# Performance work log

Measured on AMD Instinct MI355X. Metric: run time of the kernel, lower is better.

## Reference

```python
import jax, jax.numpy as jnp
from jax import lax
import numpy as np

B, F, T, D, H = 16, 20, 128, 300, 256

def _lstm_scan(x, mask, W, U, b):
    # x: [N, T, D], mask: [N, T] bool. Keras gate order: i, f, g(c), o.
    N = x.shape[0]
    xz = jnp.einsum('ntd,dh->nth', x, W) + b  # [N, T, 4H] input projection, hoisted out of scan
    def step(carry, inp):
        h, c = carry
        z_x, m = inp
        z = z_x + h @ U
        i, f, g, o = jnp.split(z, 4, axis=-1)
        c_new = jax.nn.sigmoid(f) * c + jax.nn.sigmoid(i) * jnp.tanh(g)
        h_new = jax.nn.sigmoid(o) * jnp.tanh(c_new)
        m = m[:, None]
        # Keras masking: masked steps copy previous state/output through
        h = jnp.where(m, h_new, h)
        c = jnp.where(m, c_new, c)
        return (h, c), h
    init = (jnp.zeros((N, H), x.dtype), jnp.zeros((N, H), x.dtype))
    _, hs = lax.scan(step, init, (jnp.swapaxes(xz, 0, 1), jnp.swapaxes(mask, 0, 1)))
    return jnp.swapaxes(hs, 0, 1)  # [N, T, H]

def setup_inputs() -> dict:
    key = jax.random.key(0)
    ks = jax.random.split(key, 8)
    facts = jax.random.normal(ks[0], (B, F, T, D), dtype=jnp.float32)
    lengths = jax.random.randint(ks[1], (B, F), T // 2, T + 1)
    mask = jnp.arange(T)[None, None, :] < lengths[..., None]  # valid-prefix padding mask [B,F,T]
    s_in = 1.0 / np.sqrt(D)
    s_h = 1.0 / np.sqrt(H)
    W_fwd = jax.random.normal(ks[2], (D, 4 * H), dtype=jnp.float32) * s_in
    U_fwd = jax.random.normal(ks[3], (H, 4 * H), dtype=jnp.float32) * s_h
    b_fwd = jnp.zeros((4 * H,), dtype=jnp.float32).at[H:2 * H].set(1.0)  # unit forget bias
    W_bwd = jax.random.normal(ks[4], (D, 4 * H), dtype=jnp.float32) * s_in
    U_bwd = jax.random.normal(ks[5], (H, 4 * H), dtype=jnp.float32) * s_h
    b_bwd = jnp.zeros((4 * H,), dtype=jnp.float32).at[H:2 * H].set(1.0)
    return {"facts": facts, "mask": mask, "W_fwd": W_fwd, "U_fwd": U_fwd, "b_fwd": b_fwd,
            "W_bwd": W_bwd, "U_bwd": U_bwd, "b_bwd": b_bwd}

def reference(facts, mask, W_fwd, U_fwd, b_fwd, W_bwd, U_bwd, b_bwd):
    # Flatten (B, F) -> N sequences, as in FactEncoder.call
    x = facts.reshape(B * F, T, D)
    m = mask.reshape(B * F, T)
    h_f = _lstm_scan(x, m, W_fwd, U_fwd, b_fwd)
    # Bidirectional backward branch: reverse time, run, reverse output back
    h_b = _lstm_scan(x[:, ::-1], m[:, ::-1], W_bwd, U_bwd, b_bwd)[:, ::-1]
    out = jnp.concatenate([h_f, h_b], axis=-1)  # merge_mode='concat'
    return out.reshape(B, F, T, 2 * H)
```

## Files before the change

### kernel.cpp

```cpp
#include <hip/hip_runtime.h>
#include <hip/hip_bf16.h>

constexpr int Bc   = 16;
constexpr int Fc   = 20;
constexpr int T    = 128;
constexpr int D    = 300;
constexpr int H    = 256;
constexpr int NSEQ = Bc * Fc;
constexpr int G4   = 4 * H;
constexpr int DP   = 320;

constexpr int WTN = 2 * G4 * DP;
constexpr int UTN = 2 * G4 * H;

typedef __attribute__((ext_vector_type(8))) short  short8_t;
typedef __attribute__((ext_vector_type(4))) float  f32x4;

__device__ __forceinline__ short8_t ld8(const short* p) { return *(const short8_t*)p; }
__device__ __forceinline__ f32x4 mf(short8_t a, short8_t b, f32x4 c) {
    return __builtin_amdgcn_mfma_f32_16x16x32_bf16(a, b, c, 0, 0, 0);
}
__device__ __forceinline__ float b2f(short s) {
    unsigned u = ((unsigned)(unsigned short)s) << 16;
    return __builtin_bit_cast(float, u);
}
__device__ __forceinline__ short f2b(float f) {
    unsigned u = __builtin_bit_cast(unsigned, f);
    u += 0x7fffu + ((u >> 16) & 1u);
    return (short)(u >> 16);
}
__device__ __forceinline__ float blo(unsigned w) { return __builtin_bit_cast(float, w << 16); }
__device__ __forceinline__ float bhi(unsigned w) { return __builtin_bit_cast(float, w & 0xffff0000u); }
__device__ __forceinline__ float sigf(float x) {
    float e = __builtin_amdgcn_exp2f(x * -1.44269504f);
    return __builtin_amdgcn_rcpf(1.0f + e);
}
__device__ __forceinline__ float tanhf_(float x) {
    float e = __builtin_amdgcn_exp2f(x * -2.88539008f);
    return __builtin_amdgcn_rcpf(1.0f + e) * 2.0f - 1.0f;
}
__device__ __forceinline__ bool in_is_fp32(const unsigned* bfw) {
    return bfw[256] == 0x3F800000u;
}
__device__ __forceinline__ float in_val(const void* p, long long i, bool is32) {
    return is32 ? ((const float*)p)[i] : b2f(((const short*)p)[i]);
}

__global__ void prep_wu(const void* __restrict__ Wf, const void* __restrict__ Uf,
                        const void* __restrict__ Wb, const void* __restrict__ Ub,
                        const unsigned* __restrict__ bfw,
                        short* __restrict__ wt, short* __restrict__ ut)
{
    const bool is32 = in_is_fp32(bfw);
    int idx = blockIdx.x * 256 + threadIdx.x;
    if (idx < WTN) {
        int d_ = idx / (G4 * DP), j = idx - d_ * (G4 * DP);
        int n  = j / DP, k = j - n * DP;
        const void* W = d_ ? Wb : Wf;
        wt[idx] = (k < D) ? f2b(in_val(W, (long long)k * G4 + n, is32)) : (short)0;
    } else if (idx < WTN + UTN) {
        int i  = idx - WTN;
        int d_ = i / (G4 * H), j = i - d_ * (G4 * H);
        int n  = j / H, k = j - n * H;
        const void* U = d_ ? Ub : Uf;
        int kp = (k & ~31) | ((k & 15) << 1) | ((k >> 4) & 1);
        ut[i - k + kp] = f2b(in_val(U, (long long)k * G4 + n, is32));
    }
}

__global__ void prep_xp(const void* __restrict__ facts, const unsigned* __restrict__ bfw,
                        short* __restrict__ xpc, int Tc, int t00, int t01, int ndir)
{
    const bool is32 = in_is_fp32(bfw);
    long long total = (long long)ndir * NSEQ * Tc * DP;
    long long idx = (long long)blockIdx.x * 256 + threadIdx.x;
    if (idx >= total) return;
    int perdir = NSEQ * Tc * DP;
    int d_  = (int)(idx / perdir);
    int rem = (int)(idx - (long long)d_ * perdir);
    int seq = rem / (Tc * DP);
    int r2  = rem - seq * (Tc * DP);
    int tl  = r2 / DP;
    int k   = r2 - tl * DP;
    int t0  = d_ ? t01 : t00;
    long long frow = (long long)(seq * T + t0 + tl) * D;
    xpc[idx] = (k < D) ? f2b(in_val(facts, frow + k, is32)) : (short)0;
}

__global__ void gemm_xz(const short* __restrict__ xpc, const short* __restrict__ wt,
                        const void* __restrict__ bfv, const void* __restrict__ bbv,
                        const unsigned* __restrict__ bfw,
                        short* __restrict__ xzc, int Tc, int aDirStride)
{
    const bool is32 = in_is_fp32(bfw);
    const int dir = blockIdx.z;
    const short* wtd  = wt + (size_t)dir * G4 * DP;
    const void*  bias = dir ? bbv : bfv;
    const short* xpA = xpc + (size_t)dir * aDirStride + (size_t)blockIdx.y * 128 * DP;
    short* xzd = xzc + (size_t)dir * NSEQ * Tc * G4;

    const int m0 = blockIdx.y * 128;
    const int n0 = blockIdx.x * 128;
    const int tid = threadIdx.x;
    const int wid = tid >> 6, lane = tid & 63, quad = lane >> 4, l15 = lane & 15;
    const int wm = wid >> 1, wn = wid & 1;

    __shared__ __align__(16) short Al[128 * 40];
    __shared__ __align__(16) short Bl[128 * 40];

    const short* wtB = wtd + (size_t)n0 * DP;

    const int row0 = tid >> 2,          cc0 = tid & 3;
    const int row1 = (tid + 256) >> 2,  cc1 = (tid + 256) & 3;

    f32x4 acc[4][4];
#pragma unroll
    for (int mi = 0; mi < 4; ++mi)
#pragma unroll
        for (int ni = 0; ni < 4; ++ni) acc[mi][ni] = (f32x4){0.f, 0.f, 0.f, 0.f};

    short8_t ra0, ra1, rb0, rb1;
    ra0 = ld8(xpA + (size_t)row0 * DP + cc0 * 8);
    rb0 = ld8(wtB + (size_t)row0 * DP + cc0 * 8);
    ra1 = ld8(xpA + (size_t)row1 * DP + cc1 * 8);
    rb1 = ld8(wtB + (size_t)row1 * DP + cc1 * 8);

    for (int kk = 0; kk < 10; ++kk) {
        __syncthreads();
        *(short8_t*)&Al[row0 * 40 + cc0 * 8] = ra0;
        *(short8_t*)&Bl[row0 * 40 + cc0 * 8] = rb0;
        *(short8_t*)&Al[row1 * 40 + cc1 * 8] = ra1;
        *(short8_t*)&Bl[row1 * 40 + cc1 * 8] = rb1;
        __syncthreads();

        if (kk < 9) {
            int ko = (kk + 1) * 32;
            ra0 = ld8(xpA + (size_t)row0 * DP + ko + cc0 * 8);
            rb0 = ld8(wtB + (size_t)row0 * DP + ko + cc0 * 8);
            ra1 = ld8(xpA + (size_t)row1 * DP + ko + cc1 * 8);
            rb1 = ld8(wtB + (size_t)row1 * DP + ko + cc1 * 8);
        }

        short8_t a[4], b[4];
#pragma unroll
        for (int mi = 0; mi < 4; ++mi)
            a[mi] = ld8(&Al[(wm * 64 + mi * 16 + l15) * 40 + quad * 8]);
#pragma unroll
        for (int ni = 0; ni < 4; ++ni)
            b[ni] = ld8(&Bl[(wn * 64 + ni * 16 + l15) * 40 + quad * 8]);
#pragma unroll
        for (int mi = 0; mi < 4; ++mi)
#pragma unroll
            for (int ni = 0; ni < 4; ++ni)
                acc[mi][ni] = mf(a[mi], b[ni], acc[mi][ni]);
    }

#pragma unroll
    for (int ni = 0; ni < 4; ++ni) {
        int col = n0 + wn * 64 + ni * 16 + l15;
        float bv = is32 ? ((const float*)bias)[col] : b2f(((const short*)bias)[col]);
        int pos = (col & ~31) | ((col & 15) << 1) | ((col >> 4) & 1);
#pragma unroll
        for (int mi = 0; mi < 4; ++mi) {
            int row = m0 + wm * 64 + mi * 16 + quad * 4;
#pragma unroll
            for (int r = 0; r < 4; ++r)
                xzd[(size_t)(row + r) * G4 + pos] = f2b(acc[mi][ni][r] + bv);
        }
    }
}

__global__ __launch_bounds__(512, 2)
void lstm_chunk(const short* __restrict__ xzc, const short* __restrict__ utp,
                const void* __restrict__ maskp, void* __restrict__ out,
                const unsigned* __restrict__ bfw,
                short* __restrict__ h_ws, float* __restrict__ c_ws,
                int Tc, int cbase, int first)
{
    const bool is32 = in_is_fp32(bfw);
    const int tid = threadIdx.x;
    const int wv = tid >> 6, lane = tid & 63, quad = lane >> 4, l15 = lane & 15;
    const int g = blockIdx.x;
    const int dir = g / 20, s0 = (g % 20) * 16;

    const short* ut  = utp + (size_t)dir * G4 * H;
    const short* xzd = xzc + (size_t)dir * NSEQ * Tc * G4;

    constexpr int HR = 296;
    __shared__ __align__(16) short hbuf[2][16 * HR];
    __shared__ __align__(16) short ulds[8 * 2 * 8 * 64 * 8];
    __shared__ __align__(4) unsigned char mbuf[T * 16];

    {
        const unsigned* mw = (const unsigned*)maskp;
        unsigned w0 = mw[0];
        int mode = (w0 == 1u || w0 == 0x3F800000u) ? 0 : (w0 == 0x3F803F80u ? 1 : 2);
        for (int i = tid; i < T * 16; i += 512) {
            int t = i >> 4, sq = i & 15;
            int gi = (s0 + sq) * T + t;
            unsigned char mv;
            if (mode == 0)      mv = (mw[gi] != 0) ? 1 : 0;
            else if (mode == 1) mv = (((const unsigned short*)maskp)[gi] != 0) ? 1 : 0;
            else                mv = ((const unsigned char*)maskp)[gi];
            mbuf[i] = mv;
        }
    }

    const int fb = l15 * H + quad * 8;
    const int c7 = (3 * 256 + 32 * wv + 16) * H + fb;

    short8_t ureg[5][8];
    {
        const int cr[5] = { (0*256 + 32*wv +  0) * H + fb,
                            (0*256 + 32*wv + 16) * H + fb,
                            (1*256 + 32*wv +  0) * H + fb,
                            (1*256 + 32*wv + 16) * H + fb,
                            (2*256 + 32*wv +  0) * H + fb };
#pragma unroll
        for (int a = 0; a < 5; ++a)
#pragma unroll
            for (int kk = 0; kk < 8; ++kk)
                ureg[a][kk] = ld8(ut + cr[a] + kk * 32);
    }
#pragma unroll
    for (int a = 0; a < 5; ++a)
#pragma unroll
        for (int kk = 0; kk < 8; ++kk)
            asm volatile("" : "+v"(ureg[a][kk]));

    {
        const int c5 = (2 * 256 + 32 * wv + 16) * H + fb;
        const int c6 = (3 * 256 + 32 * wv +  0) * H + fb;
#pragma unroll
        for (int kk = 0; kk < 8; ++kk) {
            *(short8_t*)&ulds[(((wv * 2 + 0) * 8 + kk) * 64 + lane) * 8] = ld8(ut + c5 + kk * 32);
            *(short8_t*)&ulds[(((wv * 2 + 1) * 8 + kk) * 64 + lane) * 8] = ld8(ut + c6 + kk * 32);
        }
    }

    for (int i = tid; i < 16 * 256; i += 512) {
        int sq = i >> 8, d = i & 255;
        int pos = (d & ~31) | ((d & 15) << 1) | ((d >> 4) & 1);
        hbuf[0][sq * HR + pos] = first ? (short)0
            : h_ws[(size_t)(dir * NSEQ + s0 + sq) * H + d];
    }
    float cst[2][4], hst[2][4];
#pragma unroll
    for (int jj = 0; jj < 2; ++jj)
#pragma unroll
        for (int r = 0; r < 4; ++r) {
            size_t sidx = (size_t)(dir * NSEQ + s0 + quad * 4 + r) * H + 32 * wv + 16 * jj + l15;
            hst[jj][r] = first ? 0.f : b2f(h_ws[sidx]);
            cst[jj][r] = first ? 0.f : c_ws[sidx];
        }

    const int dstep = dir ? -1 : 1;
    const int tl0 = dir ? (Tc - 1) : 0;
    const int tg0 = dir ? (T - 1 - cbase) : cbase;

    const unsigned* xzu = (const unsigned*)xzd;
    const int seqb = s0 + quad * 4;
    int xzo0 = (seqb * Tc + tl0) * 512 + 16 * wv + l15;
    int ob0  = (seqb * T + tg0) * (2 * H) + dir * H + 32 * wv + l15;

    short8_t u7[4];
#pragma unroll
    for (int i = 0; i < 4; ++i) u7[i] = ld8(ut + c7 + i * 32);

    unsigned xzn[4][4];
#pragma unroll
    for (int gi = 0; gi < 4; ++gi)
#pragma unroll
        for (int r = 0; r < 4; ++r)
            xzn[gi][r] = xzu[xzo0 + r * (Tc * 512) + gi * 128];

    __syncthreads();

    int p = 0;
    for (int s = 0; s < Tc; ++s) {
        const int t = dir ? (T - 1 - cbase - s) : (cbase + s);

        f32x4 acc[8];
#pragma unroll
        for (int a = 0; a < 8; ++a) acc[a] = (f32x4){0.f, 0.f, 0.f, 0.f};

        const short* hb = &hbuf[p][0];
        __builtin_amdgcn_s_setprio(1);
#pragma unroll
        for (int kk = 0; kk < 8; ++kk) {
            short8_t af = ld8(&hb[l15 * HR + kk * 32 + quad * 8]);
#pragma unroll
            for (int a = 0; a < 5; ++a) acc[a] = mf(af, ureg[a][kk], acc[a]);
            short8_t u5 = ld8(&ulds[(((wv * 2 + 0) * 8 + kk) * 64 + lane) * 8]);
            acc[5] = mf(af, u5, acc[5]);
            short8_t u6 = ld8(&ulds[(((wv * 2 + 1) * 8 + kk) * 64 + lane) * 8]);
            acc[6] = mf(af, u6, acc[6]);
            acc[7] = mf(af, u7[kk & 3], acc[7]);
            u7[kk & 3] = ld8(ut + c7 + (((kk + 4) & 7) * 32));
        }
        __builtin_amdgcn_s_setprio(0);

        const unsigned mw4 = *(const unsigned*)&mbuf[t * 16 + quad * 4];

#pragma unroll
        for (int r = 0; r < 4; ++r) {
            bool m = ((mw4 >> (8 * r)) & 0xffu) != 0;
#pragma unroll
            for (int jj = 0; jj < 2; ++jj) {
                float xi = jj ? bhi(xzn[0][r]) : blo(xzn[0][r]);
                float xf = jj ? bhi(xzn[1][r]) : blo(xzn[1][r]);
                float xg = jj ? bhi(xzn[2][r]) : blo(xzn[2][r]);
                float xo = jj ? bhi(xzn[3][r]) : blo(xzn[3][r]);
                float zi = acc[0 + jj][r] + xi;
                float zf = acc[2 + jj][r] + xf;
                float zg = acc[4 + jj][r] + xg;
                float zo = acc[6 + jj][r] + xo;
                float iv = sigf(zi), fv = sigf(zf), gv = tanhf_(zg), ov = sigf(zo);
                float cn = fv * cst[jj][r] + iv * gv;
                float hn = ov * tanhf_(cn);
                cst[jj][r] = m ? cn : cst[jj][r];
                hst[jj][r] = m ? hn : hst[jj][r];
            }
            unsigned hw = (unsigned)(unsigned short)f2b(hst[0][r])
                        | ((unsigned)(unsigned short)f2b(hst[1][r]) << 16);
            *(unsigned*)&hbuf[p ^ 1][(quad * 4 + r) * HR + 32 * wv + 2 * l15] = hw;
            int ob = ob0 + r * (T * 2 * H);
            if (is32) {
                ((float*)out)[ob]      = hst[0][r];
                ((float*)out)[ob + 16] = hst[1][r];
            } else {
                ((short*)out)[ob]      = (short)(hw & 0xffffu);
                ((short*)out)[ob + 16] = (short)(hw >> 16);
            }
        }
        xzo0 += dstep * 512;
#pragma unroll
        for (int gi = 0; gi < 4; ++gi)
#pragma unroll
            for (int r = 0; r < 4; ++r)
                xzn[gi][r] = xzu[xzo0 + r * (Tc * 512) + gi * 128];

        ob0 += dstep * 512;
        p ^= 1;
        asm volatile("s_waitcnt lgkmcnt(0)" ::: "memory");
        __builtin_amdgcn_s_barrier();
        __builtin_amdgcn_sched_barrier(0);
    }

#pragma unroll
    for (int jj = 0; jj < 2; ++jj)
#pragma unroll
        for (int r = 0; r < 4; ++r) {
            size_t sidx = (size_t)(dir * NSEQ + s0 + quad * 4 + r) * H + 32 * wv + 16 * jj + l15;
            h_ws[sidx] = f2b(hst[jj][r]);
            c_ws[sidx] = cst[jj][r];
        }
}

extern "C" void kernel_launch(void* const* d_in, const int* in_sizes, int n_in,
                              void* d_out, int out_size, void* d_ws, size_t ws_size,
                              hipStream_t stream)
{
    const void* facts = d_in[0];
    const void* maskp = d_in[1];
    const void* Wf = d_in[2];
    const void* Uf = d_in[3];
    const void* bf = d_in[4];
    const void* Wb = d_in[5];
    const void* Ub = d_in[6];
    const void* bb = d_in[7];
    const unsigned* bfw = (const unsigned*)bf;

    const unsigned long long fixedB =
        (unsigned long long)(WTN + UTN) * 2 + (2ull * NSEQ * H) * 2 + (2ull * NSEQ * H) * 4 + 1024;
    int Tc = 128;
    while (Tc > 4 && (1720320ull * Tc + fixedB) > ws_size) Tc >>= 1;
    const int nC = T / Tc;

    short* ws   = (short*)d_ws;
    short* xzc  = ws;
    short* xpc  = xzc + (size_t)2 * NSEQ * Tc * G4;
    short* wt   = xpc + (size_t)2 * NSEQ * Tc * DP;
    short* ut   = wt + WTN;
    short* h_ws = ut + UTN;
    float* c_ws = (float*)(h_ws + (size_t)2 * NSEQ * H);

    prep_wu<<<(WTN + UTN + 255) / 256, 256, 0, stream>>>(Wf, Uf, Wb, Ub, bfw, wt, ut);

    for (int c = 0; c < nC; ++c) {
        int t00 = c * Tc;
        int t01 = T - (c + 1) * Tc;
        const int ndir = (t00 == t01) ? 1 : 2;
        const int aDirStride = (t00 == t01) ? 0 : NSEQ * Tc * DP;
        const long long xpTotal = (long long)ndir * NSEQ * Tc * DP;
        prep_xp<<<(int)((xpTotal + 255) / 256), 256, 0, stream>>>(facts, bfw, xpc, Tc, t00, t01, ndir);
        gemm_xz<<<dim3(8, NSEQ * Tc / 128, 2), 256, 0, stream>>>(xpc, wt, bf, bb, bfw, xzc, Tc, aDirStride);
        lstm_chunk<<<40, 512, 0, stream>>>(xzc, ut, maskp, d_out, bfw, h_ws, c_ws,
                                           Tc, c * Tc, c == 0 ? 1 : 0);
    }
}
```

Measured before the change: 770.4 us.

## Double-buffer LDS in input-projection GEMM and pack bf16 pair stores

The input-projection GEMM now uses two LDS buffers with a prefetch distance of two k-tiles. This drops one of the two barriers per k-step and lets global loads overlap the MFMA work. The epilogue pairs adjacent interleaved columns (col and col+16) into a single 32-bit store instead of two 16-bit scattered stores, to cut store instructions. The cost is doubled LDS use and hand-written waitcnt/barrier sequencing, which can limit occupancy and carries synchronisation risk.

```diff
diff --git a/kernel.cpp b/kernel.cpp
--- a/kernel.cpp
+++ b/kernel.cpp
@@ -87,10 +87,11 @@
     xpc[idx] = (k < D) ? f2b(in_val(facts, frow + k, is32)) : (short)0;
 }
 
-__global__ void gemm_xz(const short* __restrict__ xpc, const short* __restrict__ wt,
-                        const void* __restrict__ bfv, const void* __restrict__ bbv,
-                        const unsigned* __restrict__ bfw,
-                        short* __restrict__ xzc, int Tc, int aDirStride)
+__global__ __launch_bounds__(256)
+void gemm_xz(const short* __restrict__ xpc, const short* __restrict__ wt,
+             const void* __restrict__ bfv, const void* __restrict__ bbv,
+             const unsigned* __restrict__ bfw,
+             short* __restrict__ xzc, int Tc, int aDirStride)
 {
     const bool is32 = in_is_fp32(bfw);
     const int dir = blockIdx.z;
@@ -105,13 +106,17 @@
     const int wid = tid >> 6, lane = tid & 63, quad = lane >> 4, l15 = lane & 15;
     const int wm = wid >> 1, wn = wid & 1;
 
-    __shared__ __align__(16) short Al[128 * 40];
-    __shared__ __align__(16) short Bl[128 * 40];
+    __shared__ __align__(16) short Al[2][128 * 40];
+    __shared__ __align__(16) short Bl[2][128 * 40];
 
     const short* wtB = wtd + (size_t)n0 * DP;
 
     const int row0 = tid >> 2,          cc0 = tid & 3;
     const int row1 = (tid + 256) >> 2,  cc1 = (tid + 256) & 3;
+    const size_t ga0 = (size_t)row0 * DP + cc0 * 8;
+    const size_t ga1 = (size_t)row1 * DP + cc1 * 8;
+    const int la0 = row0 * 40 + cc0 * 8;
+    const int la1 = row1 * 40 + cc1 * 8;
 
     f32x4 acc[4][4];
 #pragma unroll
@@ -119,53 +124,60 @@
 #pragma unroll
         for (int ni = 0; ni < 4; ++ni) acc[mi][ni] = (f32x4){0.f, 0.f, 0.f, 0.f};
 
-    short8_t ra0, ra1, rb0, rb1;
-    ra0 = ld8(xpA + (size_t)row0 * DP + cc0 * 8);
-    rb0 = ld8(wtB + (size_t)row0 * DP + cc0 * 8);
-    ra1 = ld8(xpA + (size_t)row1 * DP + cc1 * 8);
-    rb1 = ld8(wtB + (size_t)row1 * DP + cc1 * 8);
+    short8_t ra0 = ld8(xpA + ga0), rb0 = ld8(wtB + ga0);
+    short8_t ra1 = ld8(xpA + ga1), rb1 = ld8(wtB + ga1);
+    *(short8_t*)&Al[0][la0] = ra0;  *(short8_t*)&Bl[0][la0] = rb0;
+    *(short8_t*)&Al[0][la1] = ra1;  *(short8_t*)&Bl[0][la1] = rb1;
+    ra0 = ld8(xpA + ga0 + 32);  rb0 = ld8(wtB + ga0 + 32);
+    ra1 = ld8(xpA + ga1 + 32);  rb1 = ld8(wtB + ga1 + 32);
+    asm volatile("s_waitcnt lgkmcnt(0)" ::: "memory");
+    __builtin_amdgcn_s_barrier();
+    __builtin_amdgcn_sched_barrier(0);
 
     for (int kk = 0; kk < 10; ++kk) {
-        __syncthreads();
-        *(short8_t*)&Al[row0 * 40 + cc0 * 8] = ra0;
-        *(short8_t*)&Bl[row0 * 40 + cc0 * 8] = rb0;
-        *(short8_t*)&Al[row1 * 40 + cc1 * 8] = ra1;
-        *(short8_t*)&Bl[row1 * 40 + cc1 * 8] = rb1;
-        __syncthreads();
-
+        const int b = kk & 1;
         if (kk < 9) {
-            int ko = (kk + 1) * 32;
-            ra0 = ld8(xpA + (size_t)row0 * DP + ko + cc0 * 8);
-            rb0 = ld8(wtB + (size_t)row0 * DP + ko + cc0 * 8);
-            ra1 = ld8(xpA + (size_t)row1 * DP + ko + cc1 * 8);
-            rb1 = ld8(wtB + (size_t)row1 * DP + ko + cc1 * 8);
-        }
-
-        short8_t a[4], b[4];
+            *(short8_t*)&Al[b ^ 1][la0] = ra0;  *(short8_t*)&Bl[b ^ 1][la0] = rb0;
+            *(short8_t*)&Al[b ^ 1][la1] = ra1;  *(short8_t*)&Bl[b ^ 1][la1] = rb1;
+        }
+        if (kk < 8) {
+            const size_t ko = (size_t)(kk + 2) * 32;
+            ra0 = ld8(xpA + ga0 + ko);  rb0 = ld8(wtB + ga0 + ko);
+            ra1 = ld8(xpA + ga1 + ko);  rb1 = ld8(wtB + ga1 + ko);
+        }
+        short8_t a[4], bq[4];
 #pragma unroll
         for (int mi = 0; mi < 4; ++mi)
-            a[mi] = ld8(&Al[(wm * 64 + mi * 16 + l15) * 40 + quad * 8]);
+            a[mi] = ld8(&Al[b][(wm * 64 + mi * 16 + l15) * 40 + quad * 8]);
 #pragma unroll
         for (int ni = 0; ni < 4; ++ni)
-            b[ni] = ld8(&Bl[(wn * 64 + ni * 16 + l15) * 40 + quad * 8]);
+            bq[ni] = ld8(&Bl[b][(wn * 64 + ni * 16 + l15) * 40 + quad * 8]);
 #pragma unroll
         for (int mi = 0; mi < 4; ++mi)
 #pragma unroll
             for (int ni = 0; ni < 4; ++ni)
-                acc[mi][ni] = mf(a[mi], b[ni], acc[mi][ni]);
-    }
-
-#pragma unroll
-    for (int ni = 0; ni < 4; ++ni) {
-        int col = n0 + wn * 64 + ni * 16 + l15;
-        float bv = is32 ? ((const float*)bias)[col] : b2f(((const short*)bias)[col]);
-        int pos = (col & ~31) | ((col & 15) << 1) | ((col >> 4) & 1);
+                acc[mi][ni] = mf(a[mi], bq[ni], acc[mi][ni]);
+        asm volatile("s_waitcnt lgkmcnt(0)" ::: "memory");
+        __builtin_amdgcn_s_barrier();
+        __builtin_amdgcn_sched_barrier(0);
+    }
+
+    unsigned* xzu = (unsigned*)xzd;
+#pragma unroll
+    for (int pr = 0; pr < 2; ++pr) {
+        const int colA = n0 + wn * 64 + pr * 32 + l15;
+        const float bv0 = is32 ? ((const float*)bias)[colA]      : b2f(((const short*)bias)[colA]);
+        const float bv1 = is32 ? ((const float*)bias)[colA + 16] : b2f(((const short*)bias)[colA + 16]);
+        const int dbase = (n0 >> 1) + wn * 32 + pr * 16 + l15;
 #pragma unroll
         for (int mi = 0; mi < 4; ++mi) {
-            int row = m0 + wm * 64 + mi * 16 + quad * 4;
-#pragma unroll
-            for (int r = 0; r < 4; ++r)
-                xzd[(size_t)(row + r) * G4 + pos] = f2b(acc[mi][ni][r] + bv);
+            const int row = m0 + wm * 64 + mi * 16 + quad * 4;
+#pragma unroll
+            for (int r = 0; r < 4; ++r) {
+                unsigned w = (unsigned)(unsigned short)f2b(acc[mi][2 * pr][r] + bv0)
+                           | ((unsigned)(unsigned short)f2b(acc[mi][2 * pr + 1][r] + bv1) << 16);
+                xzu[(size_t)(row + r) * 512 + dbase] = w;
+            }
         }
     }
 }
```

New measurement: 743.6 us. 1.04x faster.
